# Optimization experiments

Measured on AMD Instinct MI355X. Metric: run time of the kernel, lower is better.

The kernel has to match this reference:

```python
import jax, jax.numpy as jnp
import numpy as np

C, PE, L, HEADS = 256, 64, 6, 4
N_GRAPHS, S = 2048, 64            # uniform graphs of S nodes -> dense batch is a reshape
N = N_GRAPHS * S                  # 131072 nodes
E = N * 4                         # 524288 edges
BN_EPS = 1e-5


def _bn(h, g, b):
    # BatchNorm1d, training-mode statistics (biased variance), affine
    m = h.mean(0)
    v = h.var(0)
    return (h - m) / jnp.sqrt(v + BN_EPS) * g + b


def setup_inputs() -> dict:
    key = jax.random.key(0)
    ks = iter(jax.random.split(key, 64))
    def rn(shape, scale=0.05):
        return jax.random.normal(next(ks), shape, dtype=jnp.float32) * scale
    x = jax.random.randint(next(ks), (N, 1), 0, 28)
    pe = jax.random.normal(next(ks), (N, 20), dtype=jnp.float32)
    epg = E // N_GRAPHS
    base = (jnp.arange(E) // epg) * S          # edges stay within their graph
    src = base + jax.random.randint(next(ks), (E,), 0, S)
    dst = base + jax.random.randint(next(ks), (E,), 0, S)
    edge_index = jnp.stack([src, dst])
    edge_attr = jax.random.randint(next(ks), (E,), 0, 4)
    batch = jnp.arange(N) // S
    return dict(
        x=x, pe=pe, edge_index=edge_index, edge_attr=edge_attr, batch=batch,
        node_emb=rn((28, C - PE), 1.0), pe_lin_w=rn((20, PE)), pe_lin_b=jnp.zeros(PE),
        pe_norm_g=jnp.ones(20), pe_norm_b=jnp.zeros(20),
        edge_emb=rn((4, C), 1.0),
        conv_w1=rn((L, C, C)), conv_b1=jnp.zeros((L, C)),
        conv_w2=rn((L, C, C)), conv_b2=jnp.zeros((L, C)),
        attn_in_w=rn((L, C, 3 * C)), attn_in_b=jnp.zeros((L, 3 * C)),
        attn_out_w=rn((L, C, C)), attn_out_b=jnp.zeros((L, C)),
        bn1_g=jnp.ones((L, C)), bn1_b=jnp.zeros((L, C)),
        bn2_g=jnp.ones((L, C)), bn2_b=jnp.zeros((L, C)),
        bn3_g=jnp.ones((L, C)), bn3_b=jnp.zeros((L, C)),
        mlp_w1=rn((L, C, 2 * C)), mlp_b1=jnp.zeros((L, 2 * C)),
        mlp_w2=rn((L, 2 * C, C)), mlp_b2=jnp.zeros((L, C)),
        head_w1=rn((C, C // 2)), head_b1=jnp.zeros(C // 2),
        head_w2=rn((C // 2, C // 4)), head_b2=jnp.zeros(C // 4),
        head_w3=rn((C // 4, 1)), head_b3=jnp.zeros(1),
    )


def reference(x, pe, edge_index, edge_attr, batch, node_emb, pe_lin_w, pe_lin_b,
              pe_norm_g, pe_norm_b, edge_emb, conv_w1, conv_b1, conv_w2, conv_b2,
              attn_in_w, attn_in_b, attn_out_w, attn_out_b,
              bn1_g, bn1_b, bn2_g, bn2_b, bn3_g, bn3_b,
              mlp_w1, mlp_b1, mlp_w2, mlp_b2,
              head_w1, head_b1, head_w2, head_b2, head_w3, head_b3):
    x_pe = _bn(pe, pe_norm_g, pe_norm_b)
    h = jnp.concatenate([node_emb[x[:, 0]], x_pe @ pe_lin_w + pe_lin_b], axis=1)  # [N, C]
    ea = edge_emb[edge_attr]                                                      # [E, C]
    src, dst = edge_index[0], edge_index[1]
    d = C // HEADS
    scale = 1.0 / jnp.sqrt(jnp.float32(d))
    for l in range(L):
        # --- local GINEConv: nn((1+eps)*x_i + sum_j relu(x_j + e_ij)), eps=0 ---
        msg = jax.nn.relu(h[src] + ea)                          # gather + add + relu
        aggr = jax.ops.segment_sum(msg, dst, num_segments=N)    # scatter-add
        z = h + aggr
        hl = jax.nn.relu(z @ conv_w1[l] + conv_b1[l]) @ conv_w2[l] + conv_b2[l]
        hl = _bn(hl + h, bn1_g[l], bn1_b[l])                    # residual + norm1
        # --- global multihead attention on dense batch [G, S, C] ---
        hd = h.reshape(N_GRAPHS, S, C)
        qkv = hd @ attn_in_w[l] + attn_in_b[l]
        q, k, v = jnp.split(qkv, 3, axis=-1)
        q = q.reshape(N_GRAPHS, S, HEADS, d).transpose(0, 2, 1, 3)
        k = k.reshape(N_GRAPHS, S, HEADS, d).transpose(0, 2, 1, 3)
        v = v.reshape(N_GRAPHS, S, HEADS, d).transpose(0, 2, 1, 3)
        a = jax.nn.softmax(jnp.einsum('ghqd,ghkd->ghqk', q, k) * scale, axis=-1)
        o = jnp.einsum('ghqk,ghkd->ghqd', a, v).transpose(0, 2, 1, 3).reshape(N_GRAPHS, S, C)
        o = (o @ attn_out_w[l] + attn_out_b[l]).reshape(N, C)
        ha = _bn(o + h, bn2_g[l], bn2_b[l])                     # residual + norm2
        # --- combine + FFN ---
        out = hl + ha
        ff = jax.nn.relu(out @ mlp_w1[l] + mlp_b1[l]) @ mlp_w2[l] + mlp_b2[l]
        h = _bn(out + ff, bn3_g[l], bn3_b[l])                   # residual + norm3
    pooled = jax.ops.segment_sum(h, batch, num_segments=N_GRAPHS)  # global_add_pool -> [G, C]
    t = jax.nn.relu(pooled @ head_w1 + head_b1)
    t = jax.nn.relu(t @ head_w2 + head_b2)
    return t @ head_w3 + head_b3                                   # [G, 1]
```

## Files before the change

### kernel.cpp

```cpp
#include <hip/hip_runtime.h>

#define N_NODES 131072
#define N_EDGES 524288
#define CCH 256
#define N_GRAPHS_ 2048
#define SEQ 64
#define LAYERS 6

typedef unsigned short US;
typedef __attribute__((ext_vector_type(8))) short v8s;
typedef __attribute__((ext_vector_type(8))) unsigned short v8us;
typedef __attribute__((ext_vector_type(4))) float v4f;

__device__ __forceinline__ float b2f(US u) { return __uint_as_float(((unsigned)u) << 16); }
__device__ __forceinline__ US f2b(float f) {
    unsigned u = __float_as_uint(f);
    return (US)((u + 0x7fff + ((u >> 16) & 1)) >> 16);
}
__device__ __forceinline__ void gload16(const US* g, US* l) {
    __builtin_amdgcn_global_load_lds(
        (const __attribute__((address_space(1))) unsigned int*)g,
        (__attribute__((address_space(3))) unsigned int*)l, 16, 0, 0);
}

__device__ float g_stats[512];
__device__ float g_aff1[512];
__device__ float g_aff2[512];
__device__ float g_aff3[512];
__device__ float g_pe[40];
__device__ float g_peaff[40];
__device__ US    g_wt[6 * 655360];
__device__ int   g_csr[N_EDGES];
__device__ int   g_off[N_GRAPHS_ * 65];

__global__ __launch_bounds__(256) void wt_k(const float* __restrict__ cw1, const float* __restrict__ cw2,
                                            const float* __restrict__ aiw, const float* __restrict__ aow,
                                            const float* __restrict__ mw1, const float* __restrict__ mw2) {
    __shared__ float t[64][65];
    int b = blockIdx.x;
    int l = b / 160, r = b % 160;
    const float* src; int ldw, ldk, ctiles; size_t doff;
    if (r < 16)      { src = cw1 + (size_t)l * 65536;  ldw = 256; ldk = 256; ctiles = 4;  doff = 0;      }
    else if (r < 32) { src = cw2 + (size_t)l * 65536;  ldw = 256; ldk = 256; ctiles = 4;  doff = 65536;  r -= 16; }
    else if (r < 80) { src = aiw + (size_t)l * 196608; ldw = 768; ldk = 256; ctiles = 12; doff = 131072; r -= 32; }
    else if (r < 96) { src = aow + (size_t)l * 65536;  ldw = 256; ldk = 256; ctiles = 4;  doff = 327680; r -= 80; }
    else if (r < 128){ src = mw1 + (size_t)l * 131072; ldw = 512; ldk = 256; ctiles = 8;  doff = 393216; r -= 96; }
    else             { src = mw2 + (size_t)l * 131072; ldw = 256; ldk = 512; ctiles = 4;  doff = 524288; r -= 128; }
    int kt = r / ctiles, ct = r % ctiles;
    int k0 = kt * 64, c0 = ct * 64;
    US* dst = g_wt + (size_t)l * 655360 + doff;
    int tid = threadIdx.x;
    int rr = tid >> 4, c4 = (tid & 15) * 4;
    #pragma unroll
    for (int j = 0; j < 4; j++) {
        float4 v = *(const float4*)(src + (size_t)(k0 + rr + j * 16) * ldw + c0 + c4);
        t[rr + j * 16][c4 + 0] = v.x; t[rr + j * 16][c4 + 1] = v.y;
        t[rr + j * 16][c4 + 2] = v.z; t[rr + j * 16][c4 + 3] = v.w;
    }
    __syncthreads();
    #pragma unroll
    for (int j = 0; j < 4; j++) {
        int crow = rr + j * 16;
        ushort4 o;
        o.x = f2b(t[c4 + 0][crow]); o.y = f2b(t[c4 + 1][crow]);
        o.z = f2b(t[c4 + 2][crow]); o.w = f2b(t[c4 + 3][crow]);
        *(ushort4*)(dst + (size_t)(c0 + crow) * ldk + k0 + c4) = o;
    }
}

__global__ __launch_bounds__(256) void csr_k(const int* __restrict__ ei,
                                             const int* __restrict__ attr) {
    __shared__ int deg[64], off[65];
    int g = blockIdx.x, tid = threadIdx.x;
    if (tid < 64) deg[tid] = 0;
    __syncthreads();
    int e = g * 256 + tid;
    int d = ei[N_EDGES + e] - g * 64;
    int slot = atomicAdd(&deg[d], 1);
    __syncthreads();
    if (tid == 0) {
        off[0] = 0;
        for (int i = 0; i < 64; i++) off[i + 1] = off[i] + deg[i];
    }
    __syncthreads();
    g_csr[g * 256 + off[d] + slot] = (ei[e] - g * 64) | (attr[e] << 6);
    if (tid < 65) g_off[g * 65 + tid] = off[tid];
}

__global__ __launch_bounds__(256) void pe_part_k(const float* __restrict__ pe) {
    __shared__ float red[240], red2[240];
    int b = blockIdx.x, tid = threadIdx.x;
    float s = 0.f, s2 = 0.f;
    if (tid < 240) {
        int ch = tid % 20, sub = tid / 20;
        size_t r0 = (size_t)b * 512;
        for (int r = sub; r < 512; r += 12) {
            float v = pe[(r0 + r) * 20 + ch];
            s += v; s2 += v * v;
        }
        red[tid] = s; red2[tid] = s2;
    }
    __syncthreads();
    if (tid < 20) {
        float ts = 0.f, ts2 = 0.f;
        #pragma unroll
        for (int sub = 0; sub < 12; sub++) { ts += red[sub * 20 + tid]; ts2 += red2[sub * 20 + tid]; }
        atomicAdd(&g_pe[tid], ts);
        atomicAdd(&g_pe[20 + tid], ts2);
    }
}

__global__ __launch_bounds__(64) void pe_fin_k(const float* __restrict__ g,
                                               const float* __restrict__ b) {
    int t = threadIdx.x;
    if (t < 20) {
        float mean = g_pe[t] / (float)N_NODES;
        float var  = g_pe[20 + t] / (float)N_NODES - mean * mean;
        float a = g[t] * rsqrtf(var + 1e-5f);
        g_peaff[t] = a;
        g_peaff[20 + t] = b[t] - mean * a;
        g_pe[t] = 0.f;
        g_pe[20 + t] = 0.f;
    }
}

__global__ __launch_bounds__(256) void embed_k(const int* __restrict__ x,
                                               const float* __restrict__ pe,
                                               const float* __restrict__ node_emb,
                                               const float* __restrict__ plw,
                                               const float* __restrict__ plb,
                                               US* __restrict__ h) {
    int n = blockIdx.x;
    int tid = threadIdx.x;
    int xi = x[n];
    float v;
    if (tid < 192) {
        v = node_emb[xi * 192 + tid];
    } else {
        int j = tid - 192;
        float s = plb[j];
        #pragma unroll
        for (int k = 0; k < 20; k++) {
            float p = pe[(size_t)n * 20 + k] * g_peaff[k] + g_peaff[20 + k];
            s += p * plw[k * 64 + j];
        }
        v = s;
    }
    h[(size_t)n * CCH + tid] = f2b(v);
}

__global__ __launch_bounds__(256) void aggr_z_k(const US* __restrict__ h,
                                                const float* __restrict__ eemb,
                                                US* __restrict__ z) {
    __shared__ US ht[64 * 264];
    __shared__ float em[4 * 260];
    __shared__ int off[65], ce[256];
    int g = blockIdx.x, tid = threadIdx.x;
    for (int v = tid; v < 2048; v += 256) {
        int row = v >> 5, seg = (v & 31) * 8;
        *(v8us*)&ht[row * 264 + seg] = *(const v8us*)(h + (size_t)(g * 64 + row) * 256 + seg);
    }
    for (int i = tid; i < 1024; i += 256)
        em[(i >> 8) * 260 + (i & 255)] = eemb[(i >> 8) * 256 + (i & 255)];
    ce[tid] = g_csr[g * 256 + tid];
    if (tid < 65) off[tid] = g_off[g * 65 + tid];
    __syncthreads();

    int dst = tid >> 2, cq = (tid & 3) * 4;
    float acc[64];
    #pragma unroll
    for (int i = 0; i < 64; i++) acc[i] = 0.f;
    int e1 = off[dst + 1];
    for (int e = off[dst]; e < e1; e++) {
        int val = ce[e];
        int src = val & 63, a = (val >> 6) & 3;
        #pragma unroll
        for (int i = 0; i < 16; i++) {
            int c = cq + i * 16;
            ushort4 hv = *(ushort4*)&ht[src * 264 + c];
            float4 ev = *(float4*)&em[a * 260 + c];
            acc[i * 4 + 0] += fmaxf(b2f(hv.x) + ev.x, 0.f);
            acc[i * 4 + 1] += fmaxf(b2f(hv.y) + ev.y, 0.f);
            acc[i * 4 + 2] += fmaxf(b2f(hv.z) + ev.z, 0.f);
            acc[i * 4 + 3] += fmaxf(b2f(hv.w) + ev.w, 0.f);
        }
    }
    US* zp = z + (size_t)(g * 64 + dst) * 256;
    #pragma unroll
    for (int i = 0; i < 16; i++) {
        int c = cq + i * 16;
        ushort4 hv = *(ushort4*)&ht[dst * 264 + c];
        ushort4 o;
        o.x = f2b(b2f(hv.x) + acc[i * 4 + 0]);
        o.y = f2b(b2f(hv.y) + acc[i * 4 + 1]);
        o.z = f2b(b2f(hv.z) + acc[i * 4 + 2]);
        o.w = f2b(b2f(hv.w) + acc[i * 4 + 3]);
        *(ushort4*)(zp + c) = o;
    }
}

template<int NG, bool STATS>
__global__ __launch_bounds__(256, 2) void gemm_mfma_k(const US* __restrict__ A,
                                                      size_t woff, int ldk,
                                                      int w0, int w1, int w2, int w3,
                                                      const float* __restrict__ bias,
                                                      const US* __restrict__ res,
                                                      US* __restrict__ Y, int mode) {
    const US* __restrict__ Wt = g_wt + woff;
    __shared__ __align__(16) char smem[16384 + 2 * NG * 4096];
    US* As0 = (US*)smem;
    US* As1 = (US*)(smem + 8192);
    US* Bs0 = (US*)(smem + 16384);
    US* Bs1 = (US*)(smem + 16384 + NG * 4096);
    float* Es = (float*)smem;

    int tid = threadIdx.x;
    size_t row0 = (size_t)blockIdx.x * 128;
    int w = tid >> 6, l = tid & 63;
    int li = l & 15, hi = l >> 4;
    int sl = hi ^ ((li >> 1) & 3);
    int srow = l >> 2, sslot = l & 3;
    int sko = (sslot ^ ((l >> 3) & 3)) * 8;

    int a_off0 = (w * 32 + li) * 32 + sl * 8;
    int a_off1 = a_off0 + 16 * 32;
    int b_off  = li * 32 + sl * 8;

    v4f acc[2][NG * 4];
    #pragma unroll
    for (int i = 0; i < 2; i++)
        #pragma unroll
        for (int t = 0; t < NG * 4; t++) acc[i][t] = (v4f){0.f, 0.f, 0.f, 0.f};

    auto stage = [&](int kc, US* Asb, US* Bsb) {
        int k0 = kc * 32;
        #pragma unroll
        for (int j = 0; j < 2; j++) {
            int q = w * 2 + j;
            gload16(A + (row0 + q * 16 + srow) * 256 + k0 + sko, Asb + q * 512);
        }
        #pragma unroll
        for (int j = 0; j < NG; j++) {
            int q = w * NG + j;
            int col = q * 16 + srow;
            int grp = col >> 6;
            int wb = (grp == 0) ? w0 : (grp == 1) ? w1 : (grp == 2) ? w2 : w3;
            gload16(Wt + (size_t)(wb + (col & 63)) * ldk + k0 + sko, Bsb + q * 512);
        }
    };

    stage(0, As0, Bs0);
    __syncthreads();
    for (int kc = 0; kc < 8; kc++) {
        US* Asc = (kc & 1) ? As1 : As0;
        US* Bsc = (kc & 1) ? Bs1 : Bs0;
        if (kc < 7) stage(kc + 1, (kc & 1) ? As0 : As1, (kc & 1) ? Bs0 : Bs1);
        v8s a0 = *(v8s*)(Asc + a_off0);
        v8s a1 = *(v8s*)(Asc + a_off1);
        #pragma unroll
        for (int t = 0; t < NG * 4; t++) {
            v8s bf = *(v8s*)(Bsc + b_off + t * 512);
            acc[0][t] = __builtin_amdgcn_mfma_f32_16x16x32_bf16(a0, bf, acc[0][t], 0, 0, 0);
            acc[1][t] = __builtin_amdgcn_mfma_f32_16x16x32_bf16(a1, bf, acc[1][t], 0, 0, 0);
        }
        __syncthreads();
    }

    int er_f = tid >> 3;
    int lcb = (tid & 7) * 8;
    float csum = 0.f, csum2 = 0.f;
    #pragma unroll
    for (int p = 0; p < 4; p++) {
        int i = p >> 1, wh = p & 1;
        if ((w >> 1) == wh) {
            int er0 = (w & 1) * 16 + hi * 4;
            #pragma unroll
            for (int t = 0; t < NG * 4; t++) {
                int grp = t >> 2;
                int wb = (grp == 0) ? w0 : (grp == 1) ? w1 : (grp == 2) ? w2 : w3;
                float bv = bias ? bias[wb + (t & 3) * 16 + li] : 0.f;
                #pragma unroll
                for (int r = 0; r < 4; r++) {
                    float v = acc[i][t][r] + bv;
                    if (mode == 1) v = fmaxf(v, 0.f);
                    Es[(er0 + r) * 260 + t * 16 + li] = v;
                }
            }
        }
        __syncthreads();
        size_t gr = row0 + (size_t)(2 * wh + (er_f >> 4)) * 32 + i * 16 + (er_f & 15);
        #pragma unroll
        for (int s = 0; s < NG; s++) {
            int c = lcb + s * 64;
            float vs[8];
            #pragma unroll
            for (int j = 0; j < 8; j++) vs[j] = Es[er_f * 260 + c + j];
            if (mode == 2) {
                v8us rv = *(const v8us*)(res + gr * 256 + c);
                #pragma unroll
                for (int j = 0; j < 8; j++) vs[j] += b2f(rv[j]);
            }
            v8us yv;
            #pragma unroll
            for (int j = 0; j < 8; j++) yv[j] = f2b(vs[j]);
            *(v8us*)(Y + gr * 256 + c) = yv;
            if constexpr (STATS) {
                #pragma unroll
                for (int j = 0; j < 8; j++) Es[er_f * 260 + c + j] = vs[j];
            }
        }
        if constexpr (STATS) {
            __syncthreads();
            float s1 = 0.f, s2 = 0.f;
            #pragma unroll 8
            for (int r2 = 0; r2 < 32; r2++) {
                float vv = Es[r2 * 260 + tid];
                s1 += vv; s2 += vv * vv;
            }
            csum += s1; csum2 += s2;
        }
        __syncthreads();
    }
    if constexpr (STATS) {
        atomicAdd(&g_stats[tid], csum);
        atomicAdd(&g_stats[CCH + tid], csum2);
    }
}

__global__ __launch_bounds__(64) void attn_k(const US* __restrict__ qkv,
                                             US* __restrict__ o) {
    __shared__ __align__(16) US Ps[64 * 72];
    __shared__ __align__(16) US Vt[64 * 72];
    int g = blockIdx.x, l = threadIdx.x;
    int li = l & 15, hi8 = (l >> 4) * 8, hi4 = (l >> 4) * 4;
    const US* base = qkv + (size_t)g * 64 * 256;

    {
        v8us vv[8];
        #pragma unroll
        for (int jv = 0; jv < 8; jv++)
            vv[jv] = *(const v8us*)(base + l * 256 + 128 + jv * 8);
        #pragma unroll
        for (int jv = 0; jv < 8; jv++)
            #pragma unroll
            for (int e = 0; e < 8; e++)
                Vt[(jv * 8 + e) * 72 + l] = vv[jv][e];
    }

    v8s Qf[4][2], Kf[4][2];
    #pragma unroll
    for (int t = 0; t < 4; t++)
        #pragma unroll
        for (int ds = 0; ds < 2; ds++) {
            Qf[t][ds] = *(const v8s*)(base + (t * 16 + li) * 256 + ds * 32 + hi8);
            Kf[t][ds] = *(const v8s*)(base + (t * 16 + li) * 256 + 64 + ds * 32 + hi8);
        }

    v4f S[4][4];
    #pragma unroll
    for (int qt = 0; qt < 4; qt++)
        #pragma unroll
        for (int kt = 0; kt < 4; kt++) {
            v4f a = (v4f){0.f, 0.f, 0.f, 0.f};
            a = __builtin_amdgcn_mfma_f32_16x16x32_bf16(Qf[qt][0], Kf[kt][0], a, 0, 0, 0);
            a = __builtin_amdgcn_mfma_f32_16x16x32_bf16(Qf[qt][1], Kf[kt][1], a, 0, 0, 0);
            S[qt][kt] = a;
        }

    #pragma unroll
    for (int qt = 0; qt < 4; qt++)
        #pragma unroll
        for (int r = 0; r < 4; r++) {
            float mx = -1e30f;
            #pragma unroll
            for (int kt = 0; kt < 4; kt++) {
                S[qt][kt][r] *= 0.125f;
                mx = fmaxf(mx, S[qt][kt][r]);
            }
            mx = fmaxf(mx, __shfl_xor(mx, 1));
            mx = fmaxf(mx, __shfl_xor(mx, 2));
            mx = fmaxf(mx, __shfl_xor(mx, 4));
            mx = fmaxf(mx, __shfl_xor(mx, 8));
            float sum = 0.f;
            #pragma unroll
            for (int kt = 0; kt < 4; kt++) {
                float e = __expf(S[qt][kt][r] - mx);
                S[qt][kt][r] = e;
                sum += e;
            }
            sum += __shfl_xor(sum, 1);
            sum += __shfl_xor(sum, 2);
            sum += __shfl_xor(sum, 4);
            sum += __shfl_xor(sum, 8);
            float inv = 1.f / sum;
            #pragma unroll
            for (int kt = 0; kt < 4; kt++)
                Ps[(qt * 16 + hi4 + r) * 72 + kt * 16 + li] = f2b(S[qt][kt][r] * inv);
        }

    v4f O[4][4];
    #pragma unroll
    for (int qt = 0; qt < 4; qt++)
        #pragma unroll
        for (int jt = 0; jt < 4; jt++) O[qt][jt] = (v4f){0.f, 0.f, 0.f, 0.f};
    #pragma unroll
    for (int ks = 0; ks < 2; ks++) {
        v8s Pf[4], Vf[4];
        #pragma unroll
        for (int qt = 0; qt < 4; qt++)
            Pf[qt] = *(v8s*)&Ps[(qt * 16 + li) * 72 + ks * 32 + hi8];
        #pragma unroll
        for (int jt = 0; jt < 4; jt++)
            Vf[jt] = *(v8s*)&Vt[(jt * 16 + li) * 72 + ks * 32 + hi8];
        #pragma unroll
        for (int qt = 0; qt < 4; qt++)
            #pragma unroll
            for (int jt = 0; jt < 4; jt++)
                O[qt][jt] = __builtin_amdgcn_mfma_f32_16x16x32_bf16(Pf[qt], Vf[jt], O[qt][jt], 0, 0, 0);
    }

    #pragma unroll
    for (int qt = 0; qt < 4; qt++)
        #pragma unroll
        for (int jt = 0; jt < 4; jt++)
            #pragma unroll
            for (int r = 0; r < 4; r++)
                Ps[(qt * 16 + hi4 + r) * 72 + jt * 16 + li] = f2b(O[qt][jt][r]);
    US* ob = o + (size_t)(g * 64 + l) * 256;
    #pragma unroll
    for (int jv = 0; jv < 8; jv++)
        *(v8us*)(ob + jv * 8) = *(v8us*)&Ps[l * 72 + jv * 8];
}

__global__ __launch_bounds__(256) void affine_k(const float* __restrict__ g,
                                                const float* __restrict__ b, int sel) {
    int c = threadIdx.x;
    float mean = g_stats[c] / (float)N_NODES;
    float var  = g_stats[CCH + c] / (float)N_NODES - mean * mean;
    float a = g[c] * rsqrtf(var + 1e-5f);
    float* dst = (sel == 0) ? g_aff1 : (sel == 1) ? g_aff2 : g_aff3;
    dst[c] = a;
    dst[CCH + c] = b[c] - mean * a;
    g_stats[c] = 0.f;
    g_stats[CCH + c] = 0.f;
}

__global__ __launch_bounds__(256) void combine_k(const US* __restrict__ y1,
                                                 const US* __restrict__ y2,
                                                 US* __restrict__ out) {
    size_t idx = (size_t)blockIdx.x * 256 + threadIdx.x;
    size_t stride = (size_t)gridDim.x * 256;
    for (; idx < (size_t)N_NODES * CCH / 8; idx += stride) {
        size_t i = idx * 8;
        int c = (int)(i & 255);
        v8us a = *(const v8us*)(y1 + i);
        v8us b = *(const v8us*)(y2 + i);
        v8us o;
        #pragma unroll
        for (int j = 0; j < 8; j++) {
            float v = b2f(a[j]) * g_aff1[c + j] + g_aff1[CCH + c + j] +
                      b2f(b[j]) * g_aff2[c + j] + g_aff2[CCH + c + j];
            o[j] = f2b(v);
        }
        *(v8us*)(out + i) = o;
    }
}

__global__ __launch_bounds__(256) void apply_k(US* __restrict__ h) {
    size_t idx = (size_t)blockIdx.x * 256 + threadIdx.x;
    size_t stride = (size_t)gridDim.x * 256;
    for (; idx < (size_t)N_NODES * CCH / 8; idx += stride) {
        size_t i = idx * 8;
        int c = (int)(i & 255);
        v8us a = *(const v8us*)(h + i);
        v8us o;
        #pragma unroll
        for (int j = 0; j < 8; j++)
            o[j] = f2b(b2f(a[j]) * g_aff3[c + j] + g_aff3[CCH + c + j]);
        *(v8us*)(h + i) = o;
    }
}

__global__ __launch_bounds__(256) void pool_k(const US* __restrict__ h,
                                              float* __restrict__ pooled) {
    int g = blockIdx.x, c = threadIdx.x;
    float s = 0.f;
    for (int ss = 0; ss < SEQ; ss++) s += b2f(h[((size_t)g * SEQ + ss) * CCH + c]);
    pooled[(size_t)g * CCH + c] = s;
}

__global__ __launch_bounds__(128) void head_k(const float* __restrict__ pooled,
                                              const float* __restrict__ w1, const float* __restrict__ b1,
                                              const float* __restrict__ w2, const float* __restrict__ b2,
                                              const float* __restrict__ w3, const float* __restrict__ b3,
                                              float* __restrict__ outp) {
    __shared__ float p[256], t1[128], t2[64];
    int g = blockIdx.x, tid = threadIdx.x;
    p[tid] = pooled[(size_t)g * CCH + tid];
    p[tid + 128] = pooled[(size_t)g * CCH + 128 + tid];
    __syncthreads();
    float s = b1[tid];
    for (int k = 0; k < 256; k++) s += p[k] * w1[k * 128 + tid];
    t1[tid] = fmaxf(s, 0.f);
    __syncthreads();
    if (tid < 64) {
        float s2 = b2[tid];
        for (int k = 0; k < 128; k++) s2 += t1[k] * w2[k * 64 + tid];
        t2[tid] = fmaxf(s2, 0.f);
    }
    __syncthreads();
    if (tid == 0) {
        float s3 = b3[0];
        for (int k = 0; k < 64; k++) s3 += t2[k] * w3[k];
        outp[g] = s3;
    }
}

extern "C" void kernel_launch(void* const* d_in, const int* in_sizes, int n_in,
                              void* d_out, int out_size, void* d_ws, size_t ws_size,
                              hipStream_t stream) {
    const int*   x         = (const int*)  d_in[0];
    const float* pe        = (const float*)d_in[1];
    const int*   ei        = (const int*)  d_in[2];
    const int*   eattr     = (const int*)  d_in[3];
    const float* node_emb  = (const float*)d_in[5];
    const float* pe_lin_w  = (const float*)d_in[6];
    const float* pe_lin_b  = (const float*)d_in[7];
    const float* pe_norm_g = (const float*)d_in[8];
    const float* pe_norm_b = (const float*)d_in[9];
    const float* edge_emb  = (const float*)d_in[10];
    const float* conv_w1   = (const float*)d_in[11];
    const float* conv_b1   = (const float*)d_in[12];
    const float* conv_w2   = (const float*)d_in[13];
    const float* conv_b2   = (const float*)d_in[14];
    const float* attn_in_w = (const float*)d_in[15];
    const float* attn_in_b = (const float*)d_in[16];
    const float* attn_out_w= (const float*)d_in[17];
    const float* attn_out_b= (const float*)d_in[18];
    const float* bn1_g     = (const float*)d_in[19];
    const float* bn1_b     = (const float*)d_in[20];
    const float* bn2_g     = (const float*)d_in[21];
    const float* bn2_b     = (const float*)d_in[22];
    const float* bn3_g     = (const float*)d_in[23];
    const float* bn3_b     = (const float*)d_in[24];
    const float* mlp_w1    = (const float*)d_in[25];
    const float* mlp_b1    = (const float*)d_in[26];
    const float* mlp_w2    = (const float*)d_in[27];
    const float* mlp_b2    = (const float*)d_in[28];
    const float* head_w1   = (const float*)d_in[29];
    const float* head_b1   = (const float*)d_in[30];
    const float* head_w2   = (const float*)d_in[31];
    const float* head_b2   = (const float*)d_in[32];
    const float* head_w3   = (const float*)d_in[33];
    const float* head_b3   = (const float*)d_in[34];
    (void)in_sizes; (void)n_in; (void)out_size; (void)ws_size;

    char* ws = (char*)d_ws;
    US* h = (US*)(ws);
    US* A = (US*)(ws + 67108864ULL);
    US* B = (US*)(ws + 134217728ULL);
    US* C = (US*)(ws + 201326592ULL);
    float* pooled = (float*)(ws + 67108864ULL);

    wt_k<<<960, 256, 0, stream>>>(conv_w1, conv_w2, attn_in_w, attn_out_w, mlp_w1, mlp_w2);
    csr_k<<<N_GRAPHS_, 256, 0, stream>>>(ei, eattr);
    pe_part_k<<<256, 256, 0, stream>>>(pe);
    pe_fin_k<<<1, 64, 0, stream>>>(pe_norm_g, pe_norm_b);
    embed_k<<<N_NODES, 256, 0, stream>>>(x, pe, node_emb, pe_lin_w, pe_lin_b, h);

    for (int l = 0; l < LAYERS; l++) {
        size_t wl = (size_t)l * 655360;

        aggr_z_k<<<N_GRAPHS_, 256, 0, stream>>>(h, edge_emb, A);
        gemm_mfma_k<4, false><<<1024, 256, 0, stream>>>(A, wl, 256, 0, 64, 128, 192,
                                                        conv_b1 + l * 256, nullptr, B, 1);
        gemm_mfma_k<4, true><<<1024, 256, 0, stream>>>(B, wl + 65536, 256, 0, 64, 128, 192,
                                                       conv_b2 + l * 256, h, C, 2);
        affine_k<<<1, 256, 0, stream>>>(bn1_g + l * 256, bn1_b + l * 256, 0);

        for (int hh = 0; hh < 4; hh++) {
            gemm_mfma_k<3, false><<<1024, 256, 0, stream>>>(h, wl + 131072, 256,
                                                            hh * 64, 256 + hh * 64, 512 + hh * 64, 0,
                                                            attn_in_b + l * 768, nullptr, A, 0);
            attn_k<<<N_GRAPHS_, 64, 0, stream>>>(A, B + hh * 64);
        }
        gemm_mfma_k<4, true><<<1024, 256, 0, stream>>>(B, wl + 327680, 256, 0, 64, 128, 192,
                                                       attn_out_b + l * 256, h, h, 2);
        affine_k<<<1, 256, 0, stream>>>(bn2_g + l * 256, bn2_b + l * 256, 1);

        combine_k<<<2048, 256, 0, stream>>>(C, h, A);
        gemm_mfma_k<4, false><<<1024, 256, 0, stream>>>(A, wl + 393216, 256, 0, 64, 128, 192,
                                                        mlp_b1 + l * 512, nullptr, B, 1);
        gemm_mfma_k<4, false><<<1024, 256, 0, stream>>>(B, wl + 524288, 512, 0, 64, 128, 192,
                                                        mlp_b2 + l * 256, A, C, 2);
        gemm_mfma_k<4, false><<<1024, 256, 0, stream>>>(A, wl + 393216, 256, 256, 320, 384, 448,
                                                        mlp_b1 + l * 512, nullptr, B, 1);
        gemm_mfma_k<4, true><<<1024, 256, 0, stream>>>(B, wl + 524288 + 256, 512, 0, 64, 128, 192,
                                                       nullptr, C, h, 2);
        affine_k<<<1, 256, 0, stream>>>(bn3_g + l * 256, bn3_b + l * 256, 2);
        apply_k<<<2048, 256, 0, stream>>>(h);
    }

    pool_k<<<N_GRAPHS_, 256, 0, stream>>>(h, pooled);
    head_k<<<N_GRAPHS_, 128, 0, stream>>>(pooled, head_w1, head_b1, head_w2, head_b2,
                                          head_w3, head_b3, (float*)d_out);
}
```

Measured before the change: 5.370 ms.

## Halve GEMM row tile to 64, raise occupancy, swizzle block order

The MFMA GEMM now computes 64 rows per block instead of 128, so each wave holds one accumulator set instead of two. Shared memory and registers per block shrink, and launch bounds go from 2 to 4 blocks per CU. Grids double to 2048 blocks, and a block-index swizzle reorders which rows each block handles. The smaller tile lowers register pressure and raises occupancy, but each weight tile is now reused over half as many rows, so weight traffic from cache goes up.

```diff
diff --git a/kernel.cpp b/kernel.cpp
--- a/kernel.cpp
+++ b/kernel.cpp
@@ -200,52 +200,51 @@
 }
 
 template<int NG, bool STATS>
-__global__ __launch_bounds__(256, 2) void gemm_mfma_k(const US* __restrict__ A,
+__global__ __launch_bounds__(256, 4) void gemm_mfma_k(const US* __restrict__ A,
                                                       size_t woff, int ldk,
                                                       int w0, int w1, int w2, int w3,
                                                       const float* __restrict__ bias,
                                                       const US* __restrict__ res,
                                                       US* __restrict__ Y, int mode) {
     const US* __restrict__ Wt = g_wt + woff;
-    __shared__ __align__(16) char smem[16384 + 2 * NG * 4096];
+    __shared__ __align__(16) char smem[8192 + 2 * NG * 4096];
     US* As0 = (US*)smem;
-    US* As1 = (US*)(smem + 8192);
-    US* Bs0 = (US*)(smem + 16384);
-    US* Bs1 = (US*)(smem + 16384 + NG * 4096);
+    US* As1 = As0 + 2048;
+    US* Bs0 = (US*)(smem + 8192);
+    US* Bs1 = Bs0 + NG * 2048;
     float* Es = (float*)smem;
+    const int NW = NG * 64 + 4;
 
     int tid = threadIdx.x;
-    size_t row0 = (size_t)blockIdx.x * 128;
+    int bid = blockIdx.x;
+    int swz = (bid & 7) * ((int)gridDim.x >> 3) + (bid >> 3);
+    size_t row0 = (size_t)swz * 64;
     int w = tid >> 6, l = tid & 63;
     int li = l & 15, hi = l >> 4;
     int sl = hi ^ ((li >> 1) & 3);
-    int srow = l >> 2, sslot = l & 3;
-    int sko = (sslot ^ ((l >> 3) & 3)) * 8;
-
-    int a_off0 = (w * 32 + li) * 32 + sl * 8;
-    int a_off1 = a_off0 + 16 * 32;
-    int b_off  = li * 32 + sl * 8;
-
-    v4f acc[2][NG * 4];
-    #pragma unroll
-    for (int i = 0; i < 2; i++)
-        #pragma unroll
-        for (int t = 0; t < NG * 4; t++) acc[i][t] = (v4f){0.f, 0.f, 0.f, 0.f};
+    int sr = l >> 2, ss = l & 3;
+
+    int a_off = (w * 16 + li) * 32 + sl * 8;
+
+    v4f acc[NG * 4];
+    #pragma unroll
+    for (int t = 0; t < NG * 4; t++) acc[t] = (v4f){0.f, 0.f, 0.f, 0.f};
+
+    int ar = w * 16 + sr;
+    int akg = (ss ^ ((ar >> 1) & 3)) * 8;
+    const US* asrc = A + (row0 + ar) * 256 + akg;
 
     auto stage = [&](int kc, US* Asb, US* Bsb) {
         int k0 = kc * 32;
-        #pragma unroll
-        for (int j = 0; j < 2; j++) {
-            int q = w * 2 + j;
-            gload16(A + (row0 + q * 16 + srow) * 256 + k0 + sko, Asb + q * 512);
-        }
+        gload16(asrc + k0, Asb + w * 512);
         #pragma unroll
         for (int j = 0; j < NG; j++) {
-            int q = w * NG + j;
-            int col = q * 16 + srow;
-            int grp = col >> 6;
+            int cu = (j * 4 + w) * 16 + sr;
+            int grp = cu >> 6;
             int wb = (grp == 0) ? w0 : (grp == 1) ? w1 : (grp == 2) ? w2 : w3;
-            gload16(Wt + (size_t)(wb + (col & 63)) * ldk + k0 + sko, Bsb + q * 512);
+            int kg = (ss ^ ((cu >> 1) & 3)) * 8;
+            gload16(Wt + (size_t)(wb + (cu & 63)) * ldk + k0 + kg,
+                    Bsb + (j * 4 + w) * 512);
         }
     };
 
@@ -255,13 +254,11 @@
         US* Asc = (kc & 1) ? As1 : As0;
         US* Bsc = (kc & 1) ? Bs1 : Bs0;
         if (kc < 7) stage(kc + 1, (kc & 1) ? As0 : As1, (kc & 1) ? Bs0 : Bs1);
-        v8s a0 = *(v8s*)(Asc + a_off0);
-        v8s a1 = *(v8s*)(Asc + a_off1);
+        v8s a0 = *(v8s*)(Asc + a_off);
         #pragma unroll
         for (int t = 0; t < NG * 4; t++) {
-            v8s bf = *(v8s*)(Bsc + b_off + t * 512);
-            acc[0][t] = __builtin_amdgcn_mfma_f32_16x16x32_bf16(a0, bf, acc[0][t], 0, 0, 0);
-            acc[1][t] = __builtin_amdgcn_mfma_f32_16x16x32_bf16(a1, bf, acc[1][t], 0, 0, 0);
+            v8s bf = *(v8s*)(Bsc + (t * 16 + li) * 32 + sl * 8);
+            acc[t] = __builtin_amdgcn_mfma_f32_16x16x32_bf16(a0, bf, acc[t], 0, 0, 0);
         }
         __syncthreads();
     }
@@ -270,9 +267,8 @@
     int lcb = (tid & 7) * 8;
     float csum = 0.f, csum2 = 0.f;
     #pragma unroll
-    for (int p = 0; p < 4; p++) {
-        int i = p >> 1, wh = p & 1;
-        if ((w >> 1) == wh) {
+    for (int p = 0; p < 2; p++) {
+        if ((w >> 1) == p) {
             int er0 = (w & 1) * 16 + hi * 4;
             #pragma unroll
             for (int t = 0; t < NG * 4; t++) {
@@ -281,20 +277,20 @@
                 float bv = bias ? bias[wb + (t & 3) * 16 + li] : 0.f;
                 #pragma unroll
                 for (int r = 0; r < 4; r++) {
-                    float v = acc[i][t][r] + bv;
+                    float v = acc[t][r] + bv;
                     if (mode == 1) v = fmaxf(v, 0.f);
-                    Es[(er0 + r) * 260 + t * 16 + li] = v;
+                    Es[(er0 + r) * NW + t * 16 + li] = v;
                 }
             }
         }
         __syncthreads();
-        size_t gr = row0 + (size_t)(2 * wh + (er_f >> 4)) * 32 + i * 16 + (er_f & 15);
+        size_t gr = row0 + p * 32 + er_f;
         #pragma unroll
         for (int s = 0; s < NG; s++) {
-            int c = lcb + s * 64;
+            int c = s * 64 + lcb;
             float vs[8];
             #pragma unroll
-            for (int j = 0; j < 8; j++) vs[j] = Es[er_f * 260 + c + j];
+            for (int j = 0; j < 8; j++) vs[j] = Es[er_f * NW + c + j];
             if (mode == 2) {
                 v8us rv = *(const v8us*)(res + gr * 256 + c);
                 #pragma unroll
@@ -306,24 +302,28 @@
             *(v8us*)(Y + gr * 256 + c) = yv;
             if constexpr (STATS) {
                 #pragma unroll
-                for (int j = 0; j < 8; j++) Es[er_f * 260 + c + j] = vs[j];
+                for (int j = 0; j < 8; j++) Es[er_f * NW + c + j] = vs[j];
             }
         }
         if constexpr (STATS) {
             __syncthreads();
-            float s1 = 0.f, s2 = 0.f;
-            #pragma unroll 8
-            for (int r2 = 0; r2 < 32; r2++) {
-                float vv = Es[r2 * 260 + tid];
-                s1 += vv; s2 += vv * vv;
+            if (tid < NG * 64) {
+                float s1 = 0.f, s2 = 0.f;
+                #pragma unroll 8
+                for (int r2 = 0; r2 < 32; r2++) {
+                    float vv = Es[r2 * NW + tid];
+                    s1 += vv; s2 += vv * vv;
+                }
+                csum += s1; csum2 += s2;
             }
-            csum += s1; csum2 += s2;
         }
         __syncthreads();
     }
     if constexpr (STATS) {
-        atomicAdd(&g_stats[tid], csum);
-        atomicAdd(&g_stats[CCH + tid], csum2);
+        if (tid < NG * 64) {
+            atomicAdd(&g_stats[tid], csum);
+            atomicAdd(&g_stats[CCH + tid], csum2);
+        }
     }
 }
 
@@ -572,30 +572,30 @@
         size_t wl = (size_t)l * 655360;
 
         aggr_z_k<<<N_GRAPHS_, 256, 0, stream>>>(h, edge_emb, A);
-        gemm_mfma_k<4, false><<<1024, 256, 0, stream>>>(A, wl, 256, 0, 64, 128, 192,
+        gemm_mfma_k<4, false><<<2048, 256, 0, stream>>>(A, wl, 256, 0, 64, 128, 192,
                                                         conv_b1 + l * 256, nullptr, B, 1);
-        gemm_mfma_k<4, true><<<1024, 256, 0, stream>>>(B, wl + 65536, 256, 0, 64, 128, 192,
+        gemm_mfma_k<4, true><<<2048, 256, 0, stream>>>(B, wl + 65536, 256, 0, 64, 128, 192,
                                                        conv_b2 + l * 256, h, C, 2);
         affine_k<<<1, 256, 0, stream>>>(bn1_g + l * 256, bn1_b + l * 256, 0);
 
         for (int hh = 0; hh < 4; hh++) {
-            gemm_mfma_k<3, false><<<1024, 256, 0, stream>>>(h, wl + 131072, 256,
+            gemm_mfma_k<3, false><<<2048, 256, 0, stream>>>(h, wl + 131072, 256,
                                                             hh * 64, 256 + hh * 64, 512 + hh * 64, 0,
                                                             attn_in_b + l * 768, nullptr, A, 0);
             attn_k<<<N_GRAPHS_, 64, 0, stream>>>(A, B + hh * 64);
         }
-        gemm_mfma_k<4, true><<<1024, 256, 0, stream>>>(B, wl + 327680, 256, 0, 64, 128, 192,
+        gemm_mfma_k<4, true><<<2048, 256, 0, stream>>>(B, wl + 327680, 256, 0, 64, 128, 192,
                                                        attn_out_b + l * 256, h, h, 2);
         affine_k<<<1, 256, 0, stream>>>(bn2_g + l * 256, bn2_b + l * 256, 1);
 
         combine_k<<<2048, 256, 0, stream>>>(C, h, A);
-        gemm_mfma_k<4, false><<<1024, 256, 0, stream>>>(A, wl + 393216, 256, 0, 64, 128, 192,
+        gemm_mfma_k<4, false><<<2048, 256, 0, stream>>>(A, wl + 393216, 256, 0, 64, 128, 192,
                                                         mlp_b1 + l * 512, nullptr, B, 1);
-        gemm_mfma_k<4, false><<<1024, 256, 0, stream>>>(B, wl + 524288, 512, 0, 64, 128, 192,
+        gemm_mfma_k<4, false><<<2048, 256, 0, stream>>>(B, wl + 524288, 512, 0, 64, 128, 192,
                                                         mlp_b2 + l * 256, A, C, 2);
-        gemm_mfma_k<4, false><<<1024, 256, 0, stream>>>(A, wl + 393216, 256, 256, 320, 384, 448,
+        gemm_mfma_k<4, false><<<2048, 256, 0, stream>>>(A, wl + 393216, 256, 256, 320, 384, 448,
                                                         mlp_b1 + l * 512, nullptr, B, 1);
-        gemm_mfma_k<4, true><<<1024, 256, 0, stream>>>(B, wl + 524288 + 256, 512, 0, 64, 128, 192,
+        gemm_mfma_k<4, true><<<2048, 256, 0, stream>>>(B, wl + 524288 + 256, 512, 0, 64, 128, 192,
                                                        nullptr, C, h, 2);
         affine_k<<<1, 256, 0, stream>>>(bn3_g + l * 256, bn3_b + l * 256, 2);
         apply_k<<<2048, 256, 0, stream>>>(h);
```

After: 5.165 ms. 3.8% less time.
